# Kernel tuning notes

Hardware: AMD Instinct MI355X
Metric: run time of the kernel (lower is better)

Reference implementation:

```python
import jax, jax.numpy as jnp
import numpy as np
import math

D_MODEL = 1024
D_HEAD = 128
B, T = 4, 4096


def setup_inputs() -> dict:
    key = jax.random.key(0)
    ks = jax.random.split(key, 7)
    x = jax.random.normal(ks[0], (B, T, D_MODEL), dtype=jnp.float32)
    # realistic RoPE tables for positions 0..T-1, d_head//2 frequencies
    half = D_HEAD // 2
    inv_freq = 1.0 / (10000.0 ** (np.arange(0, half, dtype=np.float32) / half))
    pos = np.arange(T, dtype=np.float32)
    ang = pos[:, None] * inv_freq[None, :]  # [T, half]
    cos = jnp.asarray(np.cos(ang), dtype=jnp.float32)
    sin = jnp.asarray(np.sin(ang), dtype=jnp.float32)
    scale = 1.0 / math.sqrt(D_MODEL)
    Wq = jax.random.normal(ks[1], (D_MODEL, D_HEAD), dtype=jnp.float32) * scale
    Wk = jax.random.normal(ks[2], (D_MODEL, D_HEAD), dtype=jnp.float32) * scale
    Wv = jax.random.normal(ks[3], (D_MODEL, D_HEAD), dtype=jnp.float32) * scale
    gamma = jnp.zeros((D_HEAD,), dtype=jnp.float32)
    return {"x": x, "cos": cos, "sin": sin, "Wq": Wq, "Wk": Wk, "Wv": Wv, "gamma": gamma}


def _rotary(t, cos, sin):
    # t: [B, T, d_head]; cos/sin: [T, d_head//2]
    t1 = t[..., ::2]
    t2 = t[..., 1::2]
    r1 = t1 * cos - t2 * sin
    r2 = t1 * sin + t2 * cos
    # interleave back: stack on new last axis then flatten
    return jnp.stack([r1, r2], axis=-1).reshape(t.shape)


def reference(x, cos, sin, Wq, Wk, Wv, gamma):
    d_head = Wq.shape[-1]
    Q = x @ Wq  # [B, T, d_head]
    K = x @ Wk
    V = x @ Wv
    Qr = _rotary(Q, cos, sin)
    Kr = _rotary(K, cos, sin)
    gate = jnp.exp(gamma)  # SPD gate
    Qr = Qr * gate
    Kr = Kr * gate
    scores = jnp.einsum('btd,bsd->bts', Qr, Kr) / math.sqrt(d_head)
    attn = jax.nn.softmax(scores, axis=-1)
    out = jnp.einsum('bts,bsd->btd', attn, V)
    return out
```

## Files before the change

kernel.cpp:

```cpp
#include <hip/hip_runtime.h>

typedef _Float16 h8  __attribute__((ext_vector_type(8)));
typedef float f32x16 __attribute__((ext_vector_type(16)));

#define L2E 1.4426950408889634f

__device__ __forceinline__ void gll16(const void* g, void* l) {
  __builtin_amdgcn_global_load_lds((const __attribute__((address_space(1))) void*)g,
                                   (__attribute__((address_space(3))) void*)l, 16, 0, 0);
}

__global__ void k_cvt_x(const float* __restrict__ x, _Float16* __restrict__ xh) {
  int i = (blockIdx.x * 256 + threadIdx.x) * 8;
  float4 a = *(const float4*)(x + i);
  float4 b = *(const float4*)(x + i + 4);
  h8 o;
  o[0] = (_Float16)a.x; o[1] = (_Float16)a.y; o[2] = (_Float16)a.z; o[3] = (_Float16)a.w;
  o[4] = (_Float16)b.x; o[5] = (_Float16)b.y; o[6] = (_Float16)b.z; o[7] = (_Float16)b.w;
  *(h8*)(xh + i) = o;
}

__global__ void k_cvt_w(const float* __restrict__ Wq, const float* __restrict__ Wk,
                        const float* __restrict__ Wv, _Float16* __restrict__ WT) {
  int id = blockIdx.x * 256 + threadIdx.x;
  int mat = id >> 17;
  int rem = id & 131071;
  int k = rem >> 7;
  int c = rem & 127;
  const float* W = (mat == 0) ? Wq : ((mat == 1) ? Wk : Wv);
  WT[mat * 131072 + c * 1024 + k] = (_Float16)W[rem];
}

__global__ __launch_bounds__(256, 2) void k_proj(
    const _Float16* __restrict__ xh,
    const _Float16* __restrict__ WT,
    const float* __restrict__ cosT, const float* __restrict__ sinT,
    const float* __restrict__ gamma,
    _Float16* __restrict__ Qh, _Float16* __restrict__ Kh, _Float16* __restrict__ VT) {
  __shared__ __align__(16) unsigned char lds[65536];
  const int tid = threadIdx.x;
  const int rt  = blockIdx.x & 127;
  const int mat = blockIdx.x >> 7;
  const int w = tid >> 6, lane = tid & 63;
  const int wr = w >> 1, wc = w & 1;
  const int r32 = lane & 31, h = lane >> 5;
  const int row0 = rt * 128;
  const _Float16* Wbase = WT + mat * 131072;

  auto stage = [&](int j) {
    int k0 = j * 64;
    unsigned char* xb = lds + (j & 1) * 32768;
    unsigned char* wb = xb + 16384;
#pragma unroll
    for (int ii = 0; ii < 4; ++ii) {
      int off = ii * 4096 + tid * 16;
      int r = off >> 7;
      int c = (off >> 4) & 7;
      gll16(xh + (size_t)(row0 + r) * 1024 + k0 + ((c ^ (r & 7)) * 8), xb + off);
    }
#pragma unroll
    for (int ii = 0; ii < 4; ++ii) {
      int off = ii * 4096 + tid * 16;
      int r = off >> 7;
      int c = (off >> 4) & 7;
      gll16(Wbase + (size_t)r * 1024 + k0 + ((c ^ (r & 7)) * 8), wb + off);
    }
  };

  f32x16 acc[2][2];
#pragma unroll
  for (int a_ = 0; a_ < 2; ++a_)
#pragma unroll
    for (int b_ = 0; b_ < 2; ++b_)
#pragma unroll
      for (int r = 0; r < 16; ++r) acc[a_][b_][r] = 0.f;

  stage(0);
  for (int j = 0; j < 16; ++j) {
    if (j < 15) {
      stage(j + 1);
      asm volatile("s_waitcnt vmcnt(8)\n\ts_barrier" ::: "memory");
    } else {
      asm volatile("s_waitcnt vmcnt(0)\n\ts_barrier" ::: "memory");
    }
    const _Float16* xt = (const _Float16*)(lds + (j & 1) * 32768);
    const _Float16* wt = xt + 8192;
#pragma unroll
    for (int kk = 0; kk < 4; ++kk) {
      h8 a0, a1, b0, b1;
      { int r = wr * 64 + r32;      a0 = *(const h8*)(xt + r * 64 + (((kk * 2 + h) ^ (r & 7)) * 8)); }
      { int r = wr * 64 + 32 + r32; a1 = *(const h8*)(xt + r * 64 + (((kk * 2 + h) ^ (r & 7)) * 8)); }
      { int r = wc * 64 + r32;      b0 = *(const h8*)(wt + r * 64 + (((kk * 2 + h) ^ (r & 7)) * 8)); }
      { int r = wc * 64 + 32 + r32; b1 = *(const h8*)(wt + r * 64 + (((kk * 2 + h) ^ (r & 7)) * 8)); }
      acc[0][0] = __builtin_amdgcn_mfma_f32_32x32x16_f16(a0, b0, acc[0][0], 0, 0, 0);
      acc[0][1] = __builtin_amdgcn_mfma_f32_32x32x16_f16(a0, b1, acc[0][1], 0, 0, 0);
      acc[1][0] = __builtin_amdgcn_mfma_f32_32x32x16_f16(a1, b0, acc[1][0], 0, 0, 0);
      acc[1][1] = __builtin_amdgcn_mfma_f32_32x32x16_f16(a1, b1, acc[1][1], 0, 0, 0);
    }
    asm volatile("s_waitcnt lgkmcnt(0)\n\ts_barrier" ::: "memory");
  }

#pragma unroll
  for (int mt = 0; mt < 2; ++mt)
#pragma unroll
    for (int nt = 0; nt < 2; ++nt) {
      int col = wc * 64 + nt * 32 + r32;
      f32x16 c = acc[mt][nt];
      if (mat < 2) {
        _Float16* dst = (mat == 0) ? Qh : Kh;
        float ge = expf(gamma[col]);
        float sc = (mat == 0) ? ge * 0.08838834764831845f : ge;
        int i2 = col >> 1;
#pragma unroll
        for (int rg = 0; rg < 16; ++rg) {
          int row = row0 + wr * 64 + mt * 32 + (rg & 3) + 8 * (rg >> 2) + 4 * h;
          int pos = row & 4095;
          float cv = cosT[pos * 64 + i2], sv = sinT[pos * 64 + i2];
          float val = c[rg];
          float ot = __shfl_xor(val, 1);
          float rr = (lane & 1) ? fmaf(val, cv, ot * sv) : fmaf(val, cv, -ot * sv);
          dst[(size_t)row * 128 + col] = (_Float16)(rr * sc);
        }
      } else {
#pragma unroll
        for (int g = 0; g < 4; ++g) {
          union { _Float16 hh[4]; uint2 u; } pk;
#pragma unroll
          for (int j2 = 0; j2 < 4; ++j2) pk.hh[j2] = (_Float16)c[g * 4 + j2];
          int row = row0 + wr * 64 + mt * 32 + 8 * g + 4 * h;
          *(uint2*)(VT + (size_t)col * 16384 + row) = pk.u;
        }
      }
    }
}

__global__ __launch_bounds__(512, 2) void k_attn(
    const _Float16* __restrict__ Qh, const _Float16* __restrict__ Kh,
    const _Float16* __restrict__ VT, float* __restrict__ out) {
  extern __shared__ __align__(16) unsigned char lds_raw[];
  const int tid = threadIdx.x;
  const int bid = blockIdx.x;
  const int xcd = bid & 7;
  const int b  = xcd >> 1;
  const int q0 = ((xcd & 1) + 2 * (bid >> 3)) * 64;
  const int w = tid >> 6, lane = tid & 63;
  const int wk = w >> 1, wq = w & 1;
  const int r32 = lane & 31, h = lane >> 5;

  const _Float16* qrow = Qh + (size_t)(b * 4096 + q0 + wq * 32 + r32) * 128;
  h8 qf[8];
#pragma unroll
  for (int kk = 0; kk < 8; ++kk) qf[kk] = *(const h8*)(qrow + kk * 16 + h * 8);

  f32x16 o_acc[4];
#pragma unroll
  for (int dt = 0; dt < 4; ++dt)
#pragma unroll
    for (int r = 0; r < 16; ++r) o_acc[dt][r] = 0.f;
  float mcur = -INFINITY, lsum = 0.f;

  auto stage = [&](int j) {
    int s = tid >> 7, tt = tid & 127;
    int kv0g = b * 4096 + (4 * j + s) * 32;
    unsigned char* kb = lds_raw + (s * 2 + (j & 1)) * 8192;
    unsigned char* vb = lds_raw + 65536 + (s * 2 + (j & 1)) * 8192;
    const _Float16* Ksrc = Kh + (size_t)kv0g * 128;
#pragma unroll
    for (int ii = 0; ii < 4; ++ii) {
      int off = ii * 2048 + tt * 16;
      int r = off >> 8;
      int c = (off >> 4) & 15;
      gll16(Ksrc + r * 128 + ((c ^ (r & 7)) * 8), kb + off);
    }
#pragma unroll
    for (int ii = 0; ii < 4; ++ii) {
      int off = ii * 2048 + tt * 16;
      int row = off >> 7;
      int w8 = (off >> 4) & 7;
      int par = w8 >> 2, sl = w8 & 3;
      int d = row * 2 + par;
      int kvc = sl ^ (row & 3);
      gll16(VT + (size_t)d * 16384 + kv0g + kvc * 8, vb + off);
    }
  };

  stage(0);
  for (int i = 0; i < 32; ++i) {
    if (i < 31) {
      stage(i + 1);
      asm volatile("s_waitcnt vmcnt(8)\n\ts_barrier" ::: "memory");
    } else {
      asm volatile("s_waitcnt vmcnt(0)\n\ts_barrier" ::: "memory");
    }
    const _Float16* Kt = (const _Float16*)(lds_raw + (wk * 2 + (i & 1)) * 8192);
    const _Float16* Vt = (const _Float16*)(lds_raw + 65536 + (wk * 2 + (i & 1)) * 8192);

    f32x16 st0, st1;
#pragma unroll
    for (int r = 0; r < 16; ++r) { st0[r] = 0.f; st1[r] = 0.f; }
    __builtin_amdgcn_s_setprio(1);
#pragma unroll
    for (int kk = 0; kk < 8; ++kk) {
      int slot = (kk * 2 + h) ^ (r32 & 7);
      h8 a = *(const h8*)(Kt + r32 * 128 + slot * 8);
      if (kk & 1) st1 = __builtin_amdgcn_mfma_f32_32x32x16_f16(a, qf[kk], st1, 0, 0, 0);
      else        st0 = __builtin_amdgcn_mfma_f32_32x32x16_f16(a, qf[kk], st0, 0, 0, 0);
    }
    __builtin_amdgcn_s_setprio(0);
    f32x16 st = st0 + st1;

    float pm = fmaxf(fmaxf(fmaxf(st[0], st[1]), fmaxf(st[2], st[3])),
                     fmaxf(fmaxf(st[4], st[5]), fmaxf(st[6], st[7])));
    float pm2 = fmaxf(fmaxf(fmaxf(st[8], st[9]), fmaxf(st[10], st[11])),
                      fmaxf(fmaxf(st[12], st[13]), fmaxf(st[14], st[15])));
    pm = fmaxf(pm, pm2);
    pm = fmaxf(pm, __shfl_xor(pm, 32));
    if (!__all(pm - mcur <= 8.0f)) {
      float mnew = fmaxf(mcur, pm);
      float fsc = exp2f((mcur - mnew) * L2E);
      lsum *= fsc;
#pragma unroll
      for (int dt = 0; dt < 4; ++dt) o_acc[dt] = o_acc[dt] * fsc;
      mcur = mnew;
    }
    float mn2 = mcur * L2E;
    float pv[16]; float ps = 0.f;
#pragma unroll
    for (int r = 0; r < 16; ++r) { pv[r] = exp2f(fmaf(st[r], L2E, -mn2)); ps += pv[r]; }
    ps += __shfl_xor(ps, 32);
    lsum += ps;

    unsigned int wrd[8], owd[8];
#pragma unroll
    for (int t8 = 0; t8 < 8; ++t8) {
      auto hp = __builtin_amdgcn_cvt_pkrtz(pv[2 * t8], pv[2 * t8 + 1]);
      wrd[t8] = __builtin_bit_cast(unsigned int, hp);
    }
#pragma unroll
    for (int t8 = 0; t8 < 8; ++t8) owd[t8] = (unsigned int)__shfl_xor((int)wrd[t8], 32);
    const bool hb = (h != 0);
    __builtin_amdgcn_s_setprio(1);
#pragma unroll
    for (int kvb = 0; kvb < 2; ++kvb) {
      union { unsigned int u[4]; h8 v; } pb;
      pb.u[0] = hb ? owd[4 * kvb + 2] : wrd[4 * kvb + 0];
      pb.u[1] = hb ? owd[4 * kvb + 3] : wrd[4 * kvb + 1];
      pb.u[2] = hb ? wrd[4 * kvb + 2] : owd[4 * kvb + 0];
      pb.u[3] = hb ? wrd[4 * kvb + 3] : owd[4 * kvb + 1];
#pragma unroll
      for (int dt = 0; dt < 4; ++dt) {
        int lrow = dt * 16 + (r32 >> 1);
        int sl = (kvb * 2 + h) ^ (lrow & 3);
        h8 av = *(const h8*)(Vt + lrow * 64 + (r32 & 1) * 32 + sl * 8);
        o_acc[dt] = __builtin_amdgcn_mfma_f32_32x32x16_f16(av, pb.v, o_acc[dt], 0, 0, 0);
      }
    }
    __builtin_amdgcn_s_setprio(0);
    asm volatile("s_waitcnt lgkmcnt(0)\n\ts_barrier" ::: "memory");
  }

  __syncthreads();
  float* MB = (float*)lds_raw;
  float* ML = (float*)(lds_raw + 98304);
  if (wk >= 1) {
    int si = wk - 1;
#pragma unroll
    for (int dt = 0; dt < 4; ++dt)
#pragma unroll
      for (int rg = 0; rg < 16; ++rg)
        MB[(((si * 2 + wq) * 64) + dt * 16 + rg) * 64 + lane] = o_acc[dt][rg];
    if (lane < 32) {
      ML[(si * 2 + wq) * 64 + lane] = mcur;
      ML[(si * 2 + wq) * 64 + 32 + lane] = lsum;
    }
  }
  __syncthreads();
  if (wk == 0) {
#pragma unroll
    for (int si = 0; si < 3; ++si) {
      float m1 = ML[(si * 2 + wq) * 64 + r32];
      float l1 = ML[(si * 2 + wq) * 64 + 32 + r32];
      float ms = fmaxf(mcur, m1);
      float f0 = exp2f((mcur - ms) * L2E), f1 = exp2f((m1 - ms) * L2E);
#pragma unroll
      for (int dt = 0; dt < 4; ++dt)
#pragma unroll
        for (int rg = 0; rg < 16; ++rg)
          o_acc[dt][rg] = o_acc[dt][rg] * f0 +
                          MB[(((si * 2 + wq) * 64) + dt * 16 + rg) * 64 + lane] * f1;
      lsum = lsum * f0 + l1 * f1;
      mcur = ms;
    }
    float inv = 1.0f / lsum;
#pragma unroll
    for (int dt = 0; dt < 4; ++dt) o_acc[dt] = o_acc[dt] * inv;
  }
  __syncthreads();
  float* OT = (float*)lds_raw;
  if (wk == 0) {
#pragma unroll
    for (int dt = 0; dt < 4; ++dt)
#pragma unroll
      for (int rg = 0; rg < 16; ++rg) {
        int d = dt * 32 + (rg & 3) + 8 * (rg >> 2) + 4 * h;
        OT[(wq * 32 + r32) * 129 + d] = o_acc[dt][rg];
      }
  }
  __syncthreads();
#pragma unroll
  for (int pi = 0; pi < 16; ++pi) {
    int idx = pi * 512 + tid;
    int qr = idx >> 7, c = idx & 127;
    out[(size_t)(b * 4096 + q0 + qr) * 128 + c] = OT[qr * 129 + c];
  }
}

extern "C" void kernel_launch(void* const* d_in, const int* in_sizes, int n_in,
                              void* d_out, int out_size, void* d_ws, size_t ws_size,
                              hipStream_t stream) {
  const float* x     = (const float*)d_in[0];
  const float* cosT  = (const float*)d_in[1];
  const float* sinT  = (const float*)d_in[2];
  const float* Wq    = (const float*)d_in[3];
  const float* Wk    = (const float*)d_in[4];
  const float* Wv    = (const float*)d_in[5];
  const float* gamma = (const float*)d_in[6];
  char* ws = (char*)d_ws;
  _Float16* xh = (_Float16*)(ws);
  _Float16* WT = (_Float16*)(ws + 33554432);
  _Float16* Qh = (_Float16*)(ws + 34340864);
  _Float16* Kh = (_Float16*)(ws + 38535168);
  _Float16* VT = (_Float16*)(ws + 42729472);
  float* out = (float*)d_out;

  (void)hipFuncSetAttribute(reinterpret_cast<const void*>(k_attn),
                            hipFuncAttributeMaxDynamicSharedMemorySize, 131072);

  hipLaunchKernelGGL(k_cvt_x, dim3(8192), dim3(256), 0, stream, x, xh);
  hipLaunchKernelGGL(k_cvt_w, dim3(1536), dim3(256), 0, stream, Wq, Wk, Wv, WT);
  hipLaunchKernelGGL(k_proj, dim3(384), dim3(256), 0, stream, xh, WT, cosT, sinT, gamma, Qh, Kh, VT);
  hipLaunchKernelGGL(k_attn, dim3(256), dim3(512), 131072, stream, Qh, Kh, VT, out);
}
```

Baseline: 114.2 us.

## Pre-pack K and V into MFMA fragment layout and load directly to registers

The projection kernel now writes K and V^T in a blocked layout that matches the per-lane MFMA operand order. The attention kernel drops LDS staging via global_load_lds and instead loads K and V fragments straight from global memory into registers, prefetching the next K tile during the QK MFMAs. This removes the LDS round trip and most barriers. In exchange it gives up the reuse that staging provided: each wave pair fetches its own fragments from global/L2, and register pressure rises with the kf/vf arrays at 512 threads and 2 blocks per CU.

```diff
diff --git a/kernel.cpp b/kernel.cpp
--- a/kernel.cpp
+++ b/kernel.cpp
@@ -107,7 +107,6 @@
       int col = wc * 64 + nt * 32 + r32;
       f32x16 c = acc[mt][nt];
       if (mat < 2) {
-        _Float16* dst = (mat == 0) ? Qh : Kh;
         float ge = expf(gamma[col]);
         float sc = (mat == 0) ? ge * 0.08838834764831845f : ge;
         int i2 = col >> 1;
@@ -119,7 +118,14 @@
           float val = c[rg];
           float ot = __shfl_xor(val, 1);
           float rr = (lane & 1) ? fmaf(val, cv, ot * sv) : fmaf(val, cv, -ot * sv);
-          dst[(size_t)row * 128 + col] = (_Float16)(rr * sc);
+          float v = rr * sc;
+          if (mat == 0) {
+            Qh[(size_t)row * 128 + col] = (_Float16)v;
+          } else {
+            size_t ka = (size_t)(row >> 5) * 4096 + (col >> 4) * 512 +
+                        ((col >> 3) & 1) * 256 + (row & 31) * 8 + (col & 7);
+            Kh[ka] = (_Float16)v;
+          }
         }
       } else {
 #pragma unroll
@@ -127,8 +133,11 @@
           union { _Float16 hh[4]; uint2 u; } pk;
 #pragma unroll
           for (int j2 = 0; j2 < 4; ++j2) pk.hh[j2] = (_Float16)c[g * 4 + j2];
-          int row = row0 + wr * 64 + mt * 32 + 8 * g + 4 * h;
-          *(uint2*)(VT + (size_t)col * 16384 + row) = pk.u;
+          int kv = row0 + wr * 64 + mt * 32 + 8 * g + 4 * h;
+          size_t va = (size_t)(kv >> 5) * 4096 +
+                      ((col >> 5) * 2 + ((kv >> 4) & 1)) * 512 +
+                      ((kv >> 3) & 1) * 256 + (col & 31) * 8 + (kv & 7);
+          *(uint2*)(VT + va) = pk.u;
         }
       }
     }
@@ -152,6 +161,9 @@
 #pragma unroll
   for (int kk = 0; kk < 8; ++kk) qf[kk] = *(const h8*)(qrow + kk * 16 + h * 8);
 
+  const _Float16* Kfb = Kh + (size_t)(b * 128 + wk) * 4096 + lane * 8;
+  const _Float16* Vfb = VT + (size_t)(b * 128 + wk) * 4096 + lane * 8;
+
   f32x16 o_acc[4];
 #pragma unroll
   for (int dt = 0; dt < 4; ++dt)
@@ -159,50 +171,27 @@
     for (int r = 0; r < 16; ++r) o_acc[dt][r] = 0.f;
   float mcur = -INFINITY, lsum = 0.f;
 
-  auto stage = [&](int j) {
-    int s = tid >> 7, tt = tid & 127;
-    int kv0g = b * 4096 + (4 * j + s) * 32;
-    unsigned char* kb = lds_raw + (s * 2 + (j & 1)) * 8192;
-    unsigned char* vb = lds_raw + 65536 + (s * 2 + (j & 1)) * 8192;
-    const _Float16* Ksrc = Kh + (size_t)kv0g * 128;
-#pragma unroll
-    for (int ii = 0; ii < 4; ++ii) {
-      int off = ii * 2048 + tt * 16;
-      int r = off >> 8;
-      int c = (off >> 4) & 15;
-      gll16(Ksrc + r * 128 + ((c ^ (r & 7)) * 8), kb + off);
-    }
-#pragma unroll
-    for (int ii = 0; ii < 4; ++ii) {
-      int off = ii * 2048 + tt * 16;
-      int row = off >> 7;
-      int w8 = (off >> 4) & 7;
-      int par = w8 >> 2, sl = w8 & 3;
-      int d = row * 2 + par;
-      int kvc = sl ^ (row & 3);
-      gll16(VT + (size_t)d * 16384 + kv0g + kvc * 8, vb + off);
-    }
-  };
-
-  stage(0);
+  h8 kf[8];
+#pragma unroll
+  for (int kk = 0; kk < 8; ++kk) kf[kk] = *(const h8*)(Kfb + kk * 512);
+
   for (int i = 0; i < 32; ++i) {
-    if (i < 31) {
-      stage(i + 1);
-      asm volatile("s_waitcnt vmcnt(8)\n\ts_barrier" ::: "memory");
-    } else {
-      asm volatile("s_waitcnt vmcnt(0)\n\ts_barrier" ::: "memory");
-    }
-    const _Float16* Kt = (const _Float16*)(lds_raw + (wk * 2 + (i & 1)) * 8192);
-    const _Float16* Vt = (const _Float16*)(lds_raw + 65536 + (wk * 2 + (i & 1)) * 8192);
-
+    __builtin_amdgcn_s_barrier();
+
+    const _Float16* Vcur = Vfb + (size_t)i * 16384;
+    h8 vf[8];
+#pragma unroll
+    for (int u = 0; u < 8; ++u) vf[u] = *(const h8*)(Vcur + u * 512);
+
+    const _Float16* Knext = Kfb + (size_t)(i + 1) * 16384;
     f32x16 st0, st1;
 #pragma unroll
     for (int r = 0; r < 16; ++r) { st0[r] = 0.f; st1[r] = 0.f; }
     __builtin_amdgcn_s_setprio(1);
 #pragma unroll
     for (int kk = 0; kk < 8; ++kk) {
-      int slot = (kk * 2 + h) ^ (r32 & 7);
-      h8 a = *(const h8*)(Kt + r32 * 128 + slot * 8);
+      h8 a = kf[kk];
+      if (i < 31) kf[kk] = *(const h8*)(Knext + kk * 512);
       if (kk & 1) st1 = __builtin_amdgcn_mfma_f32_32x32x16_f16(a, qf[kk], st1, 0, 0, 0);
       else        st0 = __builtin_amdgcn_mfma_f32_32x32x16_f16(a, qf[kk], st0, 0, 0, 0);
     }
@@ -248,15 +237,10 @@
       pb.u[2] = hb ? wrd[4 * kvb + 2] : owd[4 * kvb + 0];
       pb.u[3] = hb ? wrd[4 * kvb + 3] : owd[4 * kvb + 1];
 #pragma unroll
-      for (int dt = 0; dt < 4; ++dt) {
-        int lrow = dt * 16 + (r32 >> 1);
-        int sl = (kvb * 2 + h) ^ (lrow & 3);
-        h8 av = *(const h8*)(Vt + lrow * 64 + (r32 & 1) * 32 + sl * 8);
-        o_acc[dt] = __builtin_amdgcn_mfma_f32_32x32x16_f16(av, pb.v, o_acc[dt], 0, 0, 0);
-      }
+      for (int dt = 0; dt < 4; ++dt)
+        o_acc[dt] = __builtin_amdgcn_mfma_f32_32x32x16_f16(vf[dt * 2 + kvb], pb.v, o_acc[dt], 0, 0, 0);
     }
     __builtin_amdgcn_s_setprio(0);
-    asm volatile("s_waitcnt lgkmcnt(0)\n\ts_barrier" ::: "memory");
   }
 
   __syncthreads();
```

New measurement: 113.6 us. No clear change (-0.5%).
